# Kernel tuning notes

Hardware: AMD Instinct MI355X
Metric: run time of the kernel (lower is better)

The kernel has to match this reference:

```python
import jax, jax.numpy as jnp
import numpy as np
from jax import lax

# dims
BATCH, SEQ, DMODEL = 2, 2048, 1024
EXPAND, HEADDIM, DSTATE, DCONV, MLP_INNER = 2, 64, 64, 4, 4096
DIN = EXPAND * DMODEL            # 2048
NH = DIN // HEADDIM              # 32 heads
CONV_DIM = DIN + 2 * DSTATE      # x, B, C go through the depthwise conv
DPROJ = 2 * DIN + 2 * DSTATE + NH  # z, xBC, dt
EPS = 1e-5


def rmsnorm(x, w):
    return x * lax.rsqrt(jnp.mean(x * x, axis=-1, keepdims=True) + EPS) * w


def setup_inputs() -> dict:
    key = jax.random.key(0)
    ks = jax.random.split(key, 12)
    n = lambda i, shape, scale: jax.random.normal(ks[i], shape, jnp.float32) * scale
    return {
        "hidden_tokens": n(0, (BATCH, SEQ, DMODEL), 1.0),
        "W_in": n(1, (DMODEL, DPROJ), DMODEL ** -0.5),
        "conv_w": n(2, (CONV_DIM, DCONV), 0.2),
        "conv_b": jnp.zeros((CONV_DIM,), jnp.float32),
        "dt_bias": jax.random.uniform(ks[3], (NH,), jnp.float32, -4.0, -1.0),
        "A_log": jnp.log(jax.random.uniform(ks[4], (NH,), jnp.float32, 1.0, 16.0)),
        "D_param": n(5, (NH,), 1.0),
        "norm_w": jnp.ones((DIN,), jnp.float32),
        "W_out": n(6, (DIN, DMODEL), DIN ** -0.5),
        "rms_w": jnp.ones((DMODEL,), jnp.float32),
        "mlp_w1": n(7, (DMODEL, MLP_INNER), DMODEL ** -0.5),
        "mlp_b1": jnp.zeros((MLP_INNER,), jnp.float32),
        "mlp_w2": n(8, (MLP_INNER, DMODEL), MLP_INNER ** -0.5),
        "mlp_b2": jnp.zeros((DMODEL,), jnp.float32),
    }


def _mamba2(x, W_in, conv_w, conv_b, dt_bias, A_log, D_param, norm_w, W_out):
    b, l, _ = x.shape
    zxbcdt = x @ W_in                                   # (b,l,DPROJ)
    z = zxbcdt[..., :DIN]
    xBC = zxbcdt[..., DIN:DIN + CONV_DIM]
    dt = zxbcdt[..., DIN + CONV_DIM:]                   # (b,l,NH)

    # depthwise causal conv1d over sequence
    xt = jnp.pad(xBC, ((0, 0), (DCONV - 1, 0), (0, 0))).transpose(0, 2, 1)  # (b,c,l+pad)
    conv = lax.conv_general_dilated(xt, conv_w[:, None, :], (1,), "VALID",
                                    feature_group_count=CONV_DIM,
                                    dimension_numbers=("NCH", "OIH", "NCH"))
    xBC = jax.nn.silu(conv.transpose(0, 2, 1) + conv_b)  # (b,l,CONV_DIM)

    xs = xBC[..., :DIN].reshape(b, l, NH, HEADDIM)       # (b,l,h,p)
    Bc = xBC[..., DIN:DIN + DSTATE]                      # (b,l,n), ngroups=1
    Cc = xBC[..., DIN + DSTATE:]                         # (b,l,n)

    dt = jax.nn.softplus(dt + dt_bias)                   # (b,l,h)
    A = -jnp.exp(A_log)                                  # (h,)
    dA = jnp.exp(dt * A)                                 # (b,l,h)
    dtx = dt[..., None] * xs                             # (b,l,h,p)

    def step(h, inp):
        dA_t, dtx_t, B_t, C_t = inp                      # (b,h),(b,h,p),(b,n),(b,n)
        h = dA_t[..., None, None] * h + dtx_t[..., None] * B_t[:, None, None, :]
        y = jnp.einsum("bhpn,bn->bhp", h, C_t)
        return h, y

    h0 = jnp.zeros((b, NH, HEADDIM, DSTATE), x.dtype)
    _, ys = lax.scan(step, h0, (dA.transpose(1, 0, 2), dtx.transpose(1, 0, 2, 3),
                                Bc.transpose(1, 0, 2), Cc.transpose(1, 0, 2)))
    y = ys.transpose(1, 0, 2, 3) + D_param[None, None, :, None] * xs  # (b,l,h,p)
    y = y.reshape(b, l, DIN)
    y = rmsnorm(y * jax.nn.silu(z), norm_w)              # gated RMSNorm
    return y @ W_out


def reference(hidden_tokens, W_in, conv_w, conv_b, dt_bias, A_log, D_param,
              norm_w, W_out, rms_w, mlp_w1, mlp_b1, mlp_w2, mlp_b2):
    h = hidden_tokens + _mamba2(hidden_tokens, W_in, conv_w, conv_b, dt_bias,
                                A_log, D_param, norm_w, W_out)
    hn = rmsnorm(h, rms_w)
    mlp = jax.nn.silu(hn @ mlp_w1 + mlp_b1) @ mlp_w2 + mlp_b2
    return h + mlp
```

## Files before the change

### kernel.cpp

```cpp
#include <hip/hip_runtime.h>
#include <hip/hip_bf16.h>
#include <cstdint>
#include <cstddef>

#define BATCH 2
#define SEQ 2048
#define DMODEL 1024
#define DIN 2048
#define NH 32
#define HEADDIM 64
#define DSTATE 64
#define DCONV 4
#define CONV_DIM (DIN + 2 * DSTATE)
#define DPROJ (2 * DIN + 2 * DSTATE + NH)
#define MLP_INNER 4096
#define TOKENS (BATCH * SEQ)
#define EPS 1e-5f
#define Q 64
#define NCHUNK (SEQ / Q)
#define NCH (BATCH * NCHUNK * NH)
#define LSTR 72
#define NPAD_IN 4352

typedef __attribute__((ext_vector_type(8))) short short8;
typedef __attribute__((ext_vector_type(8))) __bf16 bf16x8;
typedef __attribute__((ext_vector_type(4))) float f32x4;

__device__ inline short f2bf(float f) {
    unsigned u = __builtin_bit_cast(unsigned, f);
    u = (u + 0x7FFFu + ((u >> 16) & 1u)) >> 16;
    return (short)u;
}
__device__ inline float bf2f(short s) {
    unsigned u = ((unsigned)(unsigned short)s) << 16;
    return __builtin_bit_cast(float, u);
}
__device__ inline float silu_f(float x) { return x / (1.f + __expf(-x)); }

__device__ inline bf16x8 ld_frag(const short* p) {
    short8 s = *(const short8*)p;
    return __builtin_bit_cast(bf16x8, s);
}

__device__ inline void glds16(const short* g, short* l) {
    __builtin_amdgcn_global_load_lds(
        (const __attribute__((address_space(1))) void*)g,
        (__attribute__((address_space(3))) void*)l, 16, 0, 0);
}

template <int MODE, int KT>
__global__ __launch_bounds__(256, 2) void gemm_bf16_kernel(
    const short* __restrict__ A, const short* __restrict__ BT,
    void* __restrict__ Cout, const float* __restrict__ bias,
    const float* __restrict__ res, int M, int N, int K)
{
    const int tid  = threadIdx.x;
    const int wid  = tid >> 6;
    const int lane = tid & 63;
    const int lm   = lane & 15;
    const int lg   = lane >> 4;

    const int nb  = gridDim.x * gridDim.y;
    const int bid = blockIdx.y * gridDim.x + blockIdx.x;
    const int per = nb >> 3;
    const int nid = (bid & 7) * per + (bid >> 3);
    const int m0  = (nid / gridDim.x) * 128;
    const int n0  = (nid % gridDim.x) * 128;

    __shared__ __attribute__((aligned(16))) short Al0[128 * KT];
    __shared__ __attribute__((aligned(16))) short Al1[128 * KT];
    __shared__ __attribute__((aligned(16))) short Bl0[128 * KT];
    __shared__ __attribute__((aligned(16))) short Bl1[128 * KT];

    f32x4 acc[4][4];
#pragma unroll
    for (int i = 0; i < 4; ++i)
#pragma unroll
        for (int j = 0; j < 4; ++j) acc[i][j] = {0.f, 0.f, 0.f, 0.f};

    const int wm = (wid >> 1) * 64;
    const int wn = (wid & 1) * 64;

    constexpr int lpr = KT / 8;
    constexpr int rpi = 64 / lpr;
    constexpr int nin = 32 / rpi;
    const int srow = lane / lpr;
    const int scb  = (lane % lpr) ^ (srow & (lpr - 1));
    const int scol = scb * 8;
    const short* Ag = A  + (size_t)(m0 + wid * 32 + srow) * K + scol;
    const short* Bg = BT + (size_t)(n0 + wid * 32 + srow) * K + scol;
    const int woff = wid * 32 * KT;

    const int niter = K / KT;
    {
#pragma unroll
        for (int j = 0; j < nin; ++j) {
            glds16(Ag + (size_t)j * rpi * K, Al0 + woff + j * 512);
            glds16(Bg + (size_t)j * rpi * K, Bl0 + woff + j * 512);
        }
    }

    for (int i = 0; i < niter; ++i) {
        __syncthreads();
        const short* Ac = (i & 1) ? Al1 : Al0;
        const short* Bc = (i & 1) ? Bl1 : Bl0;
        if (i + 1 < niter) {
            int kt = (i + 1) * KT;
            short* al = ((i & 1) ? Al0 : Al1) + woff;
            short* bl = ((i & 1) ? Bl0 : Bl1) + woff;
#pragma unroll
            for (int j = 0; j < nin; ++j) {
                glds16(Ag + kt + (size_t)j * rpi * K, al + j * 512);
                glds16(Bg + kt + (size_t)j * rpi * K, bl + j * 512);
            }
        }

#pragma unroll
        for (int sub = 0; sub < KT / 32; ++sub) {
            const int cb = sub * 4 + lg;
            bf16x8 af[4], bf[4];
#pragma unroll
            for (int ii = 0; ii < 4; ++ii) {
                int ar = wm + ii * 16 + lm;
                af[ii] = ld_frag(&Ac[ar * KT + ((cb ^ (ar & (lpr - 1))) * 8)]);
            }
#pragma unroll
            for (int j = 0; j < 4; ++j) {
                int br = wn + j * 16 + lm;
                bf[j] = ld_frag(&Bc[br * KT + ((cb ^ (br & (lpr - 1))) * 8)]);
            }
#pragma unroll
            for (int ii = 0; ii < 4; ++ii)
#pragma unroll
                for (int j = 0; j < 4; ++j)
                    acc[ii][j] = __builtin_amdgcn_mfma_f32_16x16x32_bf16(af[ii], bf[j], acc[ii][j], 0, 0, 0);
        }
    }

#pragma unroll
    for (int i = 0; i < 4; ++i) {
#pragma unroll
        for (int j = 0; j < 4; ++j) {
            int col = n0 + wn + j * 16 + lm;
            if (col >= N) continue;
            float bv = (MODE == 1 || MODE == 2) ? bias[col] : 0.f;
#pragma unroll
            for (int r = 0; r < 4; ++r) {
                int row = m0 + wm + i * 16 + lg * 4 + r;
                float v = acc[i][j][r];
                if (MODE == 1) {
                    ((short*)Cout)[(size_t)row * N + col] = f2bf(silu_f(v + bv));
                } else {
                    if (MODE == 2) v = v + bv + res[(size_t)row * N + col];
                    if (MODE == 3) v = v + res[(size_t)row * N + col];
                    ((float*)Cout)[(size_t)row * N + col] = v;
                }
            }
        }
    }
}

__global__ __launch_bounds__(256) void cvt_kernel(
    const float* __restrict__ src, short* __restrict__ dst, int n4)
{
    int i = (blockIdx.x * 256 + threadIdx.x);
    if (i >= n4) return;
    f32x4 v = *(const f32x4*)(src + (size_t)i * 4);
    short4 o;
    o.x = f2bf(v.x); o.y = f2bf(v.y); o.z = f2bf(v.z); o.w = f2bf(v.w);
    *(short4*)(dst + (size_t)i * 4) = o;
}

__global__ __launch_bounds__(256) void transpose_kernel(
    const float* __restrict__ src, short* __restrict__ dst, int K, int N)
{
    __shared__ float t[32][33];
    int bx = blockIdx.x, by = blockIdx.y;
    int col = threadIdx.x & 31, row8 = threadIdx.x >> 5;
    int gn = bx * 32 + col;
#pragma unroll
    for (int r = 0; r < 4; ++r) {
        int gk = by * 32 + row8 + r * 8;
        t[row8 + r * 8][col] = (gn < N) ? src[(size_t)gk * N + gn] : 0.f;
    }
    __syncthreads();
#pragma unroll
    for (int r = 0; r < 4; ++r) {
        int n = bx * 32 + row8 + r * 8;
        dst[(size_t)n * K + by * 32 + col] = f2bf(t[col][row8 + r * 8]);
    }
}

#define CTOK 8
__global__ __launch_bounds__(256) void conv_kernel(
    const float* __restrict__ zx, const float* __restrict__ cw,
    const float* __restrict__ cb, float* __restrict__ xBCc)
{
    int c4 = blockIdx.y * 256 + threadIdx.x;
    if (c4 >= CONV_DIM / 4) return;
    int c  = c4 * 4;
    int m0 = blockIdx.x * CTOK;
    int l0 = m0 & (SEQ - 1);

    const float* base = zx + (size_t)m0 * DPROJ + DIN + c;
    f32x4 win[CTOK + 3];
#pragma unroll
    for (int j = 0; j < CTOK + 3; ++j) {
        int off = j - 3;
        if (l0 + off >= 0)
            win[j] = *(const f32x4*)(base + (ptrdiff_t)off * DPROJ);
        else
            win[j] = {0.f, 0.f, 0.f, 0.f};
    }
    f32x4 w0 = *(const f32x4*)(cw + (c + 0) * DCONV);
    f32x4 w1 = *(const f32x4*)(cw + (c + 1) * DCONV);
    f32x4 w2 = *(const f32x4*)(cw + (c + 2) * DCONV);
    f32x4 w3 = *(const f32x4*)(cw + (c + 3) * DCONV);
    f32x4 bb = *(const f32x4*)(cb + c);

    float* outp = xBCc + (size_t)m0 * CONV_DIM + c;
#pragma unroll
    for (int t = 0; t < CTOK; ++t) {
        f32x4 a = {bb.x, bb.y, bb.z, bb.w};
#pragma unroll
        for (int j = 0; j < DCONV; ++j) {
            f32x4 v = win[t + j];
            a.x += v.x * w0[j];
            a.y += v.y * w1[j];
            a.z += v.z * w2[j];
            a.w += v.w * w3[j];
        }
        f32x4 o;
        o.x = silu_f(a.x); o.y = silu_f(a.y); o.z = silu_f(a.z); o.w = silu_f(a.w);
        *(f32x4*)(outp + (size_t)t * CONV_DIM) = o;
    }
}

__global__ __launch_bounds__(256) void dt_kernel(
    const float* __restrict__ zx, const float* __restrict__ dt_bias,
    const float* __restrict__ A_log, float* __restrict__ dtb, float* __restrict__ ldab)
{
    int idx = blockIdx.x * 256 + threadIdx.x;
    if (idx >= TOKENS * NH) return;
    int hh = idx & (NH - 1);
    int m  = idx >> 5;
    float v  = zx[(size_t)m * DPROJ + DIN + CONV_DIM + hh] + dt_bias[hh];
    float dt = (v > 20.f) ? v : log1pf(__expf(v));
    dtb[idx]  = dt;
    ldab[idx] = -__expf(A_log[hh]) * dt;
}

__global__ __launch_bounds__(256) void chunk_kernel(
    const float* __restrict__ xBCc, const float* __restrict__ dtb,
    const float* __restrict__ ldab, float* __restrict__ ybuf,
    float* __restrict__ Sbuf, float* __restrict__ cumdecay)
{
    int bid = blockIdx.x;
    int h = bid & 31, c = (bid >> 5) & 31, b = bid >> 10;
    int m0 = b * SEQ + c * Q;
    int tid = threadIdx.x;
    int wid = tid >> 6, lane = tid & 63, lm = lane & 15, lg = lane >> 4;

    __shared__ __attribute__((aligned(16))) short Cc[64 * LSTR];
    __shared__ __attribute__((aligned(16))) short Bb[64 * LSTR];
    __shared__ __attribute__((aligned(16))) short BwT[64 * LSTR];
    __shared__ __attribute__((aligned(16))) short Xt[64 * LSTR];
    __shared__ __attribute__((aligned(16))) short Mm[64 * LSTR];
    __shared__ float Lc[64], dtv[64];

    if (tid < 64) {
        int s = tid;
        size_t ix = (size_t)(m0 + s) * NH + h;
        float ld = ldab[ix];
        float dt = dtb[ix];
        float v = ld;
#pragma unroll
        for (int off = 1; off < 64; off <<= 1) {
            float o = __shfl_up(v, off);
            if (s >= off) v += o;
        }
        Lc[s] = v;
        dtv[s] = dt;
        cumdecay[(size_t)bid * 64 + s] = __expf(v);
    }
    {
        int row = tid >> 2, c0 = (tid & 3) * 16;
        const float* pB = xBCc + (size_t)(m0 + row) * CONV_DIM + DIN;
#pragma unroll
        for (int u = 0; u < 4; ++u) {
            f32x4 vb = *(const f32x4*)(pB + c0 + 4 * u);
            f32x4 vc = *(const f32x4*)(pB + DSTATE + c0 + 4 * u);
            short4 sb, sc;
            sb.x = f2bf(vb.x); sb.y = f2bf(vb.y); sb.z = f2bf(vb.z); sb.w = f2bf(vb.w);
            sc.x = f2bf(vc.x); sc.y = f2bf(vc.y); sc.z = f2bf(vc.z); sc.w = f2bf(vc.w);
            *(short4*)&Bb[row * LSTR + c0 + 4 * u] = sb;
            *(short4*)&Cc[row * LSTR + c0 + 4 * u] = sc;
        }
    }
    __syncthreads();
    {
        int s = tid >> 2, c0 = (tid & 3) * 16;
        float w = dtv[s];
        float w2 = __expf(Lc[63] - Lc[s]);
        const float* pX = xBCc + (size_t)(m0 + s) * CONV_DIM + h * HEADDIM;
#pragma unroll
        for (int u = 0; u < 4; ++u) {
            f32x4 v = *(const f32x4*)(pX + c0 + 4 * u);
            Xt[(c0 + 4 * u + 0) * LSTR + s] = f2bf(v.x * w);
            Xt[(c0 + 4 * u + 1) * LSTR + s] = f2bf(v.y * w);
            Xt[(c0 + 4 * u + 2) * LSTR + s] = f2bf(v.z * w);
            Xt[(c0 + 4 * u + 3) * LSTR + s] = f2bf(v.w * w);
            short4 sb = *(short4*)&Bb[s * LSTR + c0 + 4 * u];
            BwT[(c0 + 4 * u + 0) * LSTR + s] = f2bf(bf2f(sb.x) * w2);
            BwT[(c0 + 4 * u + 1) * LSTR + s] = f2bf(bf2f(sb.y) * w2);
            BwT[(c0 + 4 * u + 2) * LSTR + s] = f2bf(bf2f(sb.z) * w2);
            BwT[(c0 + 4 * u + 3) * LSTR + s] = f2bf(bf2f(sb.w) * w2);
        }
    }
    __syncthreads();

    {
        bf16x8 af[2];
#pragma unroll
        for (int kk = 0; kk < 2; ++kk)
            af[kk] = ld_frag(&Cc[(wid * 16 + lm) * LSTR + kk * 32 + lg * 8]);
#pragma unroll
        for (int j = 0; j < 4; ++j) {
            f32x4 acc = {0.f, 0.f, 0.f, 0.f};
#pragma unroll
            for (int kk = 0; kk < 2; ++kk) {
                bf16x8 bf = ld_frag(&Bb[(j * 16 + lm) * LSTR + kk * 32 + lg * 8]);
                acc = __builtin_amdgcn_mfma_f32_16x16x32_bf16(af[kk], bf, acc, 0, 0, 0);
            }
            int s = j * 16 + lm;
            float Ls = Lc[s];
#pragma unroll
            for (int r = 0; r < 4; ++r) {
                int t = wid * 16 + lg * 4 + r;
                float val = (s <= t) ? acc[r] * __expf(Lc[t] - Ls) : 0.f;
                Mm[t * LSTR + s] = f2bf(val);
            }
        }
    }
    __syncthreads();

    {
        bf16x8 am[2], aw[2];
#pragma unroll
        for (int kk = 0; kk < 2; ++kk) {
            am[kk] = ld_frag(&Mm[(wid * 16 + lm) * LSTR + kk * 32 + lg * 8]);
            aw[kk] = ld_frag(&BwT[(wid * 16 + lm) * LSTR + kk * 32 + lg * 8]);
        }
#pragma unroll
        for (int j = 0; j < 4; ++j) {
            f32x4 a1 = {0.f, 0.f, 0.f, 0.f};
            f32x4 a2 = {0.f, 0.f, 0.f, 0.f};
#pragma unroll
            for (int kk = 0; kk < 2; ++kk) {
                bf16x8 bx = ld_frag(&Xt[(j * 16 + lm) * LSTR + kk * 32 + lg * 8]);
                a1 = __builtin_amdgcn_mfma_f32_16x16x32_bf16(am[kk], bx, a1, 0, 0, 0);
                a2 = __builtin_amdgcn_mfma_f32_16x16x32_bf16(aw[kk], bx, a2, 0, 0, 0);
            }
            int p = j * 16 + lm;
#pragma unroll
            for (int r = 0; r < 4; ++r) {
                int t = wid * 16 + lg * 4 + r;
                ybuf[(size_t)(m0 + t) * DIN + h * HEADDIM + p] = a1[r];
                Sbuf[(size_t)bid * 4096 + t * 64 + p] = a2[r];
            }
        }
    }
}

__global__ __launch_bounds__(256) void state_kernel(
    float* __restrict__ SH, const float* __restrict__ cumdecay)
{
    int bh = blockIdx.x;
    int b = bh >> 5, h = bh & 31;
    int tid = threadIdx.x;
    f32x4 H[4];
#pragma unroll
    for (int u = 0; u < 4; ++u) H[u] = {0.f, 0.f, 0.f, 0.f};
    for (int c = 0; c < NCHUNK; ++c) {
        int cid = (b * NCHUNK + c) * NH + h;
        size_t base = (size_t)cid * 4096 + (size_t)tid * 16;
        float cd = cumdecay[(size_t)cid * 64 + 63];
        f32x4 s[4];
#pragma unroll
        for (int u = 0; u < 4; ++u) s[u] = *(const f32x4*)(SH + base + u * 4);
#pragma unroll
        for (int u = 0; u < 4; ++u) *(f32x4*)(SH + base + u * 4) = H[u];
#pragma unroll
        for (int u = 0; u < 4; ++u) {
            H[u].x = cd * H[u].x + s[u].x;
            H[u].y = cd * H[u].y + s[u].y;
            H[u].z = cd * H[u].z + s[u].z;
            H[u].w = cd * H[u].w + s[u].w;
        }
    }
}

__global__ __launch_bounds__(256) void inter_kernel(
    const float* __restrict__ xBCc, const float* __restrict__ Hin,
    const float* __restrict__ cumdecay, float* __restrict__ ybuf)
{
    int bid = blockIdx.x;
    int h = bid & 31, c = (bid >> 5) & 31, b = bid >> 10;
    int m0 = b * SEQ + c * Q;
    int tid = threadIdx.x;
    int wid = tid >> 6, lane = tid & 63, lm = lane & 15, lg = lane >> 4;

    __shared__ __attribute__((aligned(16))) short Cc[64 * LSTR];
    __shared__ __attribute__((aligned(16))) short HT[64 * LSTR];
    __shared__ float eLc[64];

    if (tid < 64) eLc[tid] = cumdecay[(size_t)bid * 64 + tid];
    {
        int row = tid >> 2, c0 = (tid & 3) * 16;
        const float* pC = xBCc + (size_t)(m0 + row) * CONV_DIM + DIN + DSTATE;
        const float* pH = Hin + (size_t)bid * 4096 + row * 64;
#pragma unroll
        for (int u = 0; u < 4; ++u) {
            f32x4 vc = *(const f32x4*)(pC + c0 + 4 * u);
            short4 sc;
            sc.x = f2bf(vc.x); sc.y = f2bf(vc.y); sc.z = f2bf(vc.z); sc.w = f2bf(vc.w);
            *(short4*)&Cc[row * LSTR + c0 + 4 * u] = sc;
            f32x4 vh = *(const f32x4*)(pH + c0 + 4 * u);
            HT[(c0 + 4 * u + 0) * LSTR + row] = f2bf(vh.x);
            HT[(c0 + 4 * u + 1) * LSTR + row] = f2bf(vh.y);
            HT[(c0 + 4 * u + 2) * LSTR + row] = f2bf(vh.z);
            HT[(c0 + 4 * u + 3) * LSTR + row] = f2bf(vh.w);
        }
    }
    __syncthreads();

    bf16x8 af[2];
#pragma unroll
    for (int kk = 0; kk < 2; ++kk)
        af[kk] = ld_frag(&Cc[(wid * 16 + lm) * LSTR + kk * 32 + lg * 8]);
#pragma unroll
    for (int j = 0; j < 4; ++j) {
        f32x4 acc = {0.f, 0.f, 0.f, 0.f};
#pragma unroll
        for (int kk = 0; kk < 2; ++kk) {
            bf16x8 bh_ = ld_frag(&HT[(j * 16 + lm) * LSTR + kk * 32 + lg * 8]);
            acc = __builtin_amdgcn_mfma_f32_16x16x32_bf16(af[kk], bh_, acc, 0, 0, 0);
        }
        int p = j * 16 + lm;
#pragma unroll
        for (int r = 0; r < 4; ++r) {
            int t = wid * 16 + lg * 4 + r;
            size_t ya = (size_t)(m0 + t) * DIN + h * HEADDIM + p;
            ybuf[ya] += eLc[t] * acc[r];
        }
    }
}

__global__ __launch_bounds__(256) void norm1_kernel(
    const float* __restrict__ zx, const float* __restrict__ xBCc,
    const float* __restrict__ Dp, const float* __restrict__ y,
    short* __restrict__ ybf, const float* __restrict__ w)
{
    int m = blockIdx.x;
    int t = threadIdx.x;
    const float* zr = zx + (size_t)m * DPROJ;
    const float* xr = xBCc + (size_t)m * CONV_DIM;
    const float* yr = y + (size_t)m * DIN;
    float vals[8];
    float ss = 0.f;
#pragma unroll
    for (int j = 0; j < 8; ++j) {
        int i = j * 256 + t;
        float v = (yr[i] + Dp[i >> 6] * xr[i]) * silu_f(zr[i]);
        vals[j] = v;
        ss += v * v;
    }
#pragma unroll
    for (int o = 32; o >= 1; o >>= 1) ss += __shfl_xor(ss, o);
    __shared__ float wsum[4];
    if ((t & 63) == 0) wsum[t >> 6] = ss;
    __syncthreads();
    float tot = wsum[0] + wsum[1] + wsum[2] + wsum[3];
    float scale = rsqrtf(tot / (float)DIN + EPS);
#pragma unroll
    for (int j = 0; j < 8; ++j) {
        int i = j * 256 + t;
        ybf[(size_t)m * DIN + i] = f2bf(vals[j] * scale * w[i]);
    }
}

__global__ __launch_bounds__(256) void norm2_kernel(
    const float* __restrict__ hb, short* __restrict__ hnbf, const float* __restrict__ w)
{
    int m = blockIdx.x;
    int t = threadIdx.x;
    const float* hr = hb + (size_t)m * DMODEL;
    float vals[4];
    float ss = 0.f;
#pragma unroll
    for (int j = 0; j < 4; ++j) {
        int i = j * 256 + t;
        float v = hr[i];
        vals[j] = v;
        ss += v * v;
    }
#pragma unroll
    for (int o = 32; o >= 1; o >>= 1) ss += __shfl_xor(ss, o);
    __shared__ float wsum[4];
    if ((t & 63) == 0) wsum[t >> 6] = ss;
    __syncthreads();
    float tot = wsum[0] + wsum[1] + wsum[2] + wsum[3];
    float scale = rsqrtf(tot / (float)DMODEL + EPS);
#pragma unroll
    for (int j = 0; j < 4; ++j) {
        int i = j * 256 + t;
        hnbf[(size_t)m * DMODEL + i] = f2bf(vals[j] * scale * w[i]);
    }
}

extern "C" void kernel_launch(void* const* d_in, const int* in_sizes, int n_in,
                              void* d_out, int out_size, void* d_ws, size_t ws_size,
                              hipStream_t stream) {
    const float* x       = (const float*)d_in[0];
    const float* W_in    = (const float*)d_in[1];
    const float* conv_w  = (const float*)d_in[2];
    const float* conv_b  = (const float*)d_in[3];
    const float* dt_bias = (const float*)d_in[4];
    const float* A_log   = (const float*)d_in[5];
    const float* D_param = (const float*)d_in[6];
    const float* norm_w  = (const float*)d_in[7];
    const float* W_out   = (const float*)d_in[8];
    const float* rms_w   = (const float*)d_in[9];
    const float* mlp_w1  = (const float*)d_in[10];
    const float* mlp_b1  = (const float*)d_in[11];
    const float* mlp_w2  = (const float*)d_in[12];
    const float* mlp_b2  = (const float*)d_in[13];
    float* out = (float*)d_out;

    float* ws       = (float*)d_ws;
    float* zx       = ws;
    float* xBCc     = zx + (size_t)TOKENS * DPROJ;
    float* dtb      = xBCc + (size_t)TOKENS * CONV_DIM;
    float* ldab     = dtb + (size_t)TOKENS * NH;
    float* cumdecay = ldab + (size_t)TOKENS * NH;
    float* ybuf     = cumdecay + (size_t)TOKENS * NH;
    float* SH       = ybuf + (size_t)TOKENS * DIN;
    float* bfarea   = SH + (size_t)NCH * 4096;

    short* xbf   = (short*)ybuf;
    short* midbf = (short*)ybuf;
    float* hbuf  = SH;
    short* hnbf  = (short*)(SH + (size_t)TOKENS * DMODEL);

    short* ybf   = (short*)bfarea;
    short* WinT  = ybf + (size_t)TOKENS * DIN;
    short* WoutT = WinT + (size_t)NPAD_IN * DMODEL;
    short* w1T   = WoutT + (size_t)DMODEL * DIN;
    short* w2T   = w1T + (size_t)MLP_INNER * DMODEL;

    dim3 blk(256);

    cvt_kernel<<<dim3(TOKENS * DMODEL / 4 / 256), blk, 0, stream>>>(x, xbf, TOKENS * DMODEL / 4);
    transpose_kernel<<<dim3(NPAD_IN / 32, DMODEL / 32), blk, 0, stream>>>(W_in, WinT, DMODEL, DPROJ);
    transpose_kernel<<<dim3(DMODEL / 32, DIN / 32), blk, 0, stream>>>(W_out, WoutT, DIN, DMODEL);
    transpose_kernel<<<dim3(MLP_INNER / 32, DMODEL / 32), blk, 0, stream>>>(mlp_w1, w1T, DMODEL, MLP_INNER);
    transpose_kernel<<<dim3(DMODEL / 32, MLP_INNER / 32), blk, 0, stream>>>(mlp_w2, w2T, MLP_INNER, DMODEL);

    gemm_bf16_kernel<0, 32><<<dim3(NPAD_IN / 128, TOKENS / 128), blk, 0, stream>>>(
        xbf, WinT, zx, nullptr, nullptr, TOKENS, DPROJ, DMODEL);
    conv_kernel<<<dim3(TOKENS / CTOK, (CONV_DIM / 4 + 255) / 256), blk, 0, stream>>>(
        zx, conv_w, conv_b, xBCc);
    dt_kernel<<<dim3(TOKENS * NH / 256), blk, 0, stream>>>(zx, dt_bias, A_log, dtb, ldab);
    chunk_kernel<<<dim3(NCH), blk, 0, stream>>>(xBCc, dtb, ldab, ybuf, SH, cumdecay);
    state_kernel<<<dim3(BATCH * NH), blk, 0, stream>>>(SH, cumdecay);
    inter_kernel<<<dim3(NCH), blk, 0, stream>>>(xBCc, SH, cumdecay, ybuf);
    norm1_kernel<<<dim3(TOKENS), blk, 0, stream>>>(zx, xBCc, D_param, ybuf, ybf, norm_w);
    gemm_bf16_kernel<3, 64><<<dim3(DMODEL / 128, TOKENS / 128), blk, 0, stream>>>(
        ybf, WoutT, hbuf, nullptr, x, TOKENS, DMODEL, DIN);
    norm2_kernel<<<dim3(TOKENS), blk, 0, stream>>>(hbuf, hnbf, rms_w);
    gemm_bf16_kernel<1, 32><<<dim3(MLP_INNER / 128, TOKENS / 128), blk, 0, stream>>>(
        hnbf, w1T, midbf, mlp_b1, nullptr, TOKENS, MLP_INNER, DMODEL);
    gemm_bf16_kernel<2, 64><<<dim3(DMODEL / 128, TOKENS / 128), blk, 0, stream>>>(
        midbf, w2T, out, mlp_b2, hbuf, TOKENS, DMODEL, MLP_INNER);
}
```

Baseline: 444.8 us.

## Store in-projection and conv outputs as bf16 instead of fp32

The in-projection GEMM gets a new epilogue mode that writes bf16. The conv output buffer is also stored as bf16, and the conv, dt, chunk, inter and norm1 kernels now read these bf16 buffers directly, which removes some fp32-to-bf16 conversions in chunk and inter. The goal is to halve the memory traffic for the large intermediate activations. Separately, launch bounds now request 4 waves per SIMD for the KT=32 GEMMs, which may force register spilling. Storing z, dt and the conv outputs in bf16 lowers precision; dt in particular feeds the exponential decay.

```diff
diff --git a/kernel.cpp b/kernel.cpp
--- a/kernel.cpp
+++ b/kernel.cpp
@@ -49,7 +49,7 @@
 }
 
 template <int MODE, int KT>
-__global__ __launch_bounds__(256, 2) void gemm_bf16_kernel(
+__global__ __launch_bounds__(256, (KT == 32) ? 4 : 2) void gemm_bf16_kernel(
     const short* __restrict__ A, const short* __restrict__ BT,
     void* __restrict__ Cout, const float* __restrict__ bias,
     const float* __restrict__ res, int M, int N, int K)
@@ -150,6 +150,8 @@
                 float v = acc[i][j][r];
                 if (MODE == 1) {
                     ((short*)Cout)[(size_t)row * N + col] = f2bf(silu_f(v + bv));
+                } else if (MODE == 4) {
+                    ((short*)Cout)[(size_t)row * N + col] = f2bf(v);
                 } else {
                     if (MODE == 2) v = v + bv + res[(size_t)row * N + col];
                     if (MODE == 3) v = v + res[(size_t)row * N + col];
@@ -193,8 +195,8 @@
 
 #define CTOK 8
 __global__ __launch_bounds__(256) void conv_kernel(
-    const float* __restrict__ zx, const float* __restrict__ cw,
-    const float* __restrict__ cb, float* __restrict__ xBCc)
+    const short* __restrict__ zx, const float* __restrict__ cw,
+    const float* __restrict__ cb, short* __restrict__ xBCc)
 {
     int c4 = blockIdx.y * 256 + threadIdx.x;
     if (c4 >= CONV_DIM / 4) return;
@@ -202,15 +204,17 @@
     int m0 = blockIdx.x * CTOK;
     int l0 = m0 & (SEQ - 1);
 
-    const float* base = zx + (size_t)m0 * DPROJ + DIN + c;
+    const short* base = zx + (size_t)m0 * DPROJ + DIN + c;
     f32x4 win[CTOK + 3];
 #pragma unroll
     for (int j = 0; j < CTOK + 3; ++j) {
         int off = j - 3;
-        if (l0 + off >= 0)
-            win[j] = *(const f32x4*)(base + (ptrdiff_t)off * DPROJ);
-        else
+        if (l0 + off >= 0) {
+            short4 sv = *(const short4*)(base + (ptrdiff_t)off * DPROJ);
+            win[j] = {bf2f(sv.x), bf2f(sv.y), bf2f(sv.z), bf2f(sv.w)};
+        } else {
             win[j] = {0.f, 0.f, 0.f, 0.f};
+        }
     }
     f32x4 w0 = *(const f32x4*)(cw + (c + 0) * DCONV);
     f32x4 w1 = *(const f32x4*)(cw + (c + 1) * DCONV);
@@ -218,7 +222,7 @@
     f32x4 w3 = *(const f32x4*)(cw + (c + 3) * DCONV);
     f32x4 bb = *(const f32x4*)(cb + c);
 
-    float* outp = xBCc + (size_t)m0 * CONV_DIM + c;
+    short* outp = xBCc + (size_t)m0 * CONV_DIM + c;
 #pragma unroll
     for (int t = 0; t < CTOK; ++t) {
         f32x4 a = {bb.x, bb.y, bb.z, bb.w};
@@ -230,28 +234,29 @@
             a.z += v.z * w2[j];
             a.w += v.w * w3[j];
         }
-        f32x4 o;
-        o.x = silu_f(a.x); o.y = silu_f(a.y); o.z = silu_f(a.z); o.w = silu_f(a.w);
-        *(f32x4*)(outp + (size_t)t * CONV_DIM) = o;
+        short4 o;
+        o.x = f2bf(silu_f(a.x)); o.y = f2bf(silu_f(a.y));
+        o.z = f2bf(silu_f(a.z)); o.w = f2bf(silu_f(a.w));
+        *(short4*)(outp + (size_t)t * CONV_DIM) = o;
     }
 }
 
 __global__ __launch_bounds__(256) void dt_kernel(
-    const float* __restrict__ zx, const float* __restrict__ dt_bias,
+    const short* __restrict__ zx, const float* __restrict__ dt_bias,
     const float* __restrict__ A_log, float* __restrict__ dtb, float* __restrict__ ldab)
 {
     int idx = blockIdx.x * 256 + threadIdx.x;
     if (idx >= TOKENS * NH) return;
     int hh = idx & (NH - 1);
     int m  = idx >> 5;
-    float v  = zx[(size_t)m * DPROJ + DIN + CONV_DIM + hh] + dt_bias[hh];
+    float v  = bf2f(zx[(size_t)m * DPROJ + DIN + CONV_DIM + hh]) + dt_bias[hh];
     float dt = (v > 20.f) ? v : log1pf(__expf(v));
     dtb[idx]  = dt;
     ldab[idx] = -__expf(A_log[hh]) * dt;
 }
 
 __global__ __launch_bounds__(256) void chunk_kernel(
-    const float* __restrict__ xBCc, const float* __restrict__ dtb,
+    const short* __restrict__ xBCc, const float* __restrict__ dtb,
     const float* __restrict__ ldab, float* __restrict__ ybuf,
     float* __restrict__ Sbuf, float* __restrict__ cumdecay)
 {
@@ -285,16 +290,13 @@
     }
     {
         int row = tid >> 2, c0 = (tid & 3) * 16;
-        const float* pB = xBCc + (size_t)(m0 + row) * CONV_DIM + DIN;
-#pragma unroll
-        for (int u = 0; u < 4; ++u) {
-            f32x4 vb = *(const f32x4*)(pB + c0 + 4 * u);
-            f32x4 vc = *(const f32x4*)(pB + DSTATE + c0 + 4 * u);
-            short4 sb, sc;
-            sb.x = f2bf(vb.x); sb.y = f2bf(vb.y); sb.z = f2bf(vb.z); sb.w = f2bf(vb.w);
-            sc.x = f2bf(vc.x); sc.y = f2bf(vc.y); sc.z = f2bf(vc.z); sc.w = f2bf(vc.w);
-            *(short4*)&Bb[row * LSTR + c0 + 4 * u] = sb;
-            *(short4*)&Cc[row * LSTR + c0 + 4 * u] = sc;
+        const short* pB = xBCc + (size_t)(m0 + row) * CONV_DIM + DIN;
+#pragma unroll
+        for (int u = 0; u < 2; ++u) {
+            short8 vb = *(const short8*)(pB + c0 + 8 * u);
+            short8 vc = *(const short8*)(pB + DSTATE + c0 + 8 * u);
+            *(short8*)&Bb[row * LSTR + c0 + 8 * u] = vb;
+            *(short8*)&Cc[row * LSTR + c0 + 8 * u] = vc;
         }
     }
     __syncthreads();
@@ -302,14 +304,14 @@
         int s = tid >> 2, c0 = (tid & 3) * 16;
         float w = dtv[s];
         float w2 = __expf(Lc[63] - Lc[s]);
-        const float* pX = xBCc + (size_t)(m0 + s) * CONV_DIM + h * HEADDIM;
+        const short* pX = xBCc + (size_t)(m0 + s) * CONV_DIM + h * HEADDIM;
 #pragma unroll
         for (int u = 0; u < 4; ++u) {
-            f32x4 v = *(const f32x4*)(pX + c0 + 4 * u);
-            Xt[(c0 + 4 * u + 0) * LSTR + s] = f2bf(v.x * w);
-            Xt[(c0 + 4 * u + 1) * LSTR + s] = f2bf(v.y * w);
-            Xt[(c0 + 4 * u + 2) * LSTR + s] = f2bf(v.z * w);
-            Xt[(c0 + 4 * u + 3) * LSTR + s] = f2bf(v.w * w);
+            short4 v = *(const short4*)(pX + c0 + 4 * u);
+            Xt[(c0 + 4 * u + 0) * LSTR + s] = f2bf(bf2f(v.x) * w);
+            Xt[(c0 + 4 * u + 1) * LSTR + s] = f2bf(bf2f(v.y) * w);
+            Xt[(c0 + 4 * u + 2) * LSTR + s] = f2bf(bf2f(v.z) * w);
+            Xt[(c0 + 4 * u + 3) * LSTR + s] = f2bf(bf2f(v.w) * w);
             short4 sb = *(short4*)&Bb[s * LSTR + c0 + 4 * u];
             BwT[(c0 + 4 * u + 0) * LSTR + s] = f2bf(bf2f(sb.x) * w2);
             BwT[(c0 + 4 * u + 1) * LSTR + s] = f2bf(bf2f(sb.y) * w2);
@@ -401,7 +403,7 @@
 }
 
 __global__ __launch_bounds__(256) void inter_kernel(
-    const float* __restrict__ xBCc, const float* __restrict__ Hin,
+    const short* __restrict__ xBCc, const float* __restrict__ Hin,
     const float* __restrict__ cumdecay, float* __restrict__ ybuf)
 {
     int bid = blockIdx.x;
@@ -417,14 +419,15 @@
     if (tid < 64) eLc[tid] = cumdecay[(size_t)bid * 64 + tid];
     {
         int row = tid >> 2, c0 = (tid & 3) * 16;
-        const float* pC = xBCc + (size_t)(m0 + row) * CONV_DIM + DIN + DSTATE;
+        const short* pC = xBCc + (size_t)(m0 + row) * CONV_DIM + DIN + DSTATE;
+#pragma unroll
+        for (int u = 0; u < 2; ++u) {
+            short8 vc = *(const short8*)(pC + c0 + 8 * u);
+            *(short8*)&Cc[row * LSTR + c0 + 8 * u] = vc;
+        }
         const float* pH = Hin + (size_t)bid * 4096 + row * 64;
 #pragma unroll
         for (int u = 0; u < 4; ++u) {
-            f32x4 vc = *(const f32x4*)(pC + c0 + 4 * u);
-            short4 sc;
-            sc.x = f2bf(vc.x); sc.y = f2bf(vc.y); sc.z = f2bf(vc.z); sc.w = f2bf(vc.w);
-            *(short4*)&Cc[row * LSTR + c0 + 4 * u] = sc;
             f32x4 vh = *(const f32x4*)(pH + c0 + 4 * u);
             HT[(c0 + 4 * u + 0) * LSTR + row] = f2bf(vh.x);
             HT[(c0 + 4 * u + 1) * LSTR + row] = f2bf(vh.y);
@@ -457,21 +460,21 @@
 }
 
 __global__ __launch_bounds__(256) void norm1_kernel(
-    const float* __restrict__ zx, const float* __restrict__ xBCc,
+    const short* __restrict__ zx, const short* __restrict__ xBCc,
     const float* __restrict__ Dp, const float* __restrict__ y,
     short* __restrict__ ybf, const float* __restrict__ w)
 {
     int m = blockIdx.x;
     int t = threadIdx.x;
-    const float* zr = zx + (size_t)m * DPROJ;
-    const float* xr = xBCc + (size_t)m * CONV_DIM;
+    const short* zr = zx + (size_t)m * DPROJ;
+    const short* xr = xBCc + (size_t)m * CONV_DIM;
     const float* yr = y + (size_t)m * DIN;
     float vals[8];
     float ss = 0.f;
 #pragma unroll
     for (int j = 0; j < 8; ++j) {
         int i = j * 256 + t;
-        float v = (yr[i] + Dp[i >> 6] * xr[i]) * silu_f(zr[i]);
+        float v = (yr[i] + Dp[i >> 6] * bf2f(xr[i])) * silu_f(bf2f(zr[i]));
         vals[j] = v;
         ss += v * v;
     }
@@ -538,15 +541,17 @@
     float* out = (float*)d_out;
 
     float* ws       = (float*)d_ws;
-    float* zx       = ws;
-    float* xBCc     = zx + (size_t)TOKENS * DPROJ;
-    float* dtb      = xBCc + (size_t)TOKENS * CONV_DIM;
+    float* zxf      = ws;
+    float* xBCf     = zxf + (size_t)TOKENS * DPROJ;
+    float* dtb      = xBCf + (size_t)TOKENS * CONV_DIM;
     float* ldab     = dtb + (size_t)TOKENS * NH;
     float* cumdecay = ldab + (size_t)TOKENS * NH;
     float* ybuf     = cumdecay + (size_t)TOKENS * NH;
     float* SH       = ybuf + (size_t)TOKENS * DIN;
     float* bfarea   = SH + (size_t)NCH * 4096;
 
+    short* zxb   = (short*)zxf;
+    short* xBCb  = (short*)xBCf;
     short* xbf   = (short*)ybuf;
     short* midbf = (short*)ybuf;
     float* hbuf  = SH;
@@ -566,15 +571,15 @@
     transpose_kernel<<<dim3(MLP_INNER / 32, DMODEL / 32), blk, 0, stream>>>(mlp_w1, w1T, DMODEL, MLP_INNER);
     transpose_kernel<<<dim3(DMODEL / 32, MLP_INNER / 32), blk, 0, stream>>>(mlp_w2, w2T, MLP_INNER, DMODEL);
 
-    gemm_bf16_kernel<0, 32><<<dim3(NPAD_IN / 128, TOKENS / 128), blk, 0, stream>>>(
-        xbf, WinT, zx, nullptr, nullptr, TOKENS, DPROJ, DMODEL);
+    gemm_bf16_kernel<4, 32><<<dim3(NPAD_IN / 128, TOKENS / 128), blk, 0, stream>>>(
+        xbf, WinT, zxb, nullptr, nullptr, TOKENS, DPROJ, DMODEL);
     conv_kernel<<<dim3(TOKENS / CTOK, (CONV_DIM / 4 + 255) / 256), blk, 0, stream>>>(
-        zx, conv_w, conv_b, xBCc);
-    dt_kernel<<<dim3(TOKENS * NH / 256), blk, 0, stream>>>(zx, dt_bias, A_log, dtb, ldab);
-    chunk_kernel<<<dim3(NCH), blk, 0, stream>>>(xBCc, dtb, ldab, ybuf, SH, cumdecay);
+        zxb, conv_w, conv_b, xBCb);
+    dt_kernel<<<dim3(TOKENS * NH / 256), blk, 0, stream>>>(zxb, dt_bias, A_log, dtb, ldab);
+    chunk_kernel<<<dim3(NCH), blk, 0, stream>>>(xBCb, dtb, ldab, ybuf, SH, cumdecay);
     state_kernel<<<dim3(BATCH * NH), blk, 0, stream>>>(SH, cumdecay);
-    inter_kernel<<<dim3(NCH), blk, 0, stream>>>(xBCc, SH, cumdecay, ybuf);
-    norm1_kernel<<<dim3(TOKENS), blk, 0, stream>>>(zx, xBCc, D_param, ybuf, ybf, norm_w);
+    inter_kernel<<<dim3(NCH), blk, 0, stream>>>(xBCb, SH, cumdecay, ybuf);
+    norm1_kernel<<<dim3(TOKENS), blk, 0, stream>>>(zxb, xBCb, D_param, ybuf, ybf, norm_w);
     gemm_bf16_kernel<3, 64><<<dim3(DMODEL / 128, TOKENS / 128), blk, 0, stream>>>(
         ybf, WoutT, hbuf, nullptr, x, TOKENS, DMODEL, DIN);
     norm2_kernel<<<dim3(TOKENS), blk, 0, stream>>>(hbuf, hnbf, rms_w);
```

Result: faster. 428.7 us (-3.6%).
